# Optimization experiments

Hardware: AMD Instinct MI355X
Metric: run time of the kernel (lower is better)

## Reference

```python
import jax, jax.numpy as jnp
import numpy as np

N = 50000
E = 800000
IN_DIM = 128
OUT_DIM = 128


def setup_inputs() -> dict:
    key = jax.random.key(0)
    k1, k2, k3, k4 = jax.random.split(key, 4)
    x = jax.random.normal(k1, (N, IN_DIM), dtype=jnp.float32)
    edge_index = jax.random.randint(k2, (2, E), 0, N, dtype=jnp.int64)
    # Linear(in_dim*2, out_dim) params
    W = jax.random.normal(k3, (2 * IN_DIM, OUT_DIM), dtype=jnp.float32) * (1.0 / np.sqrt(2 * IN_DIM))
    b = jax.random.normal(k4, (OUT_DIM,), dtype=jnp.float32) * 0.01
    return {"x": x, "edge_index": edge_index, "W": W, "b": b}


def reference(x, edge_index, W, b):
    src, dst = edge_index[0], edge_index[1]
    diff = x[src] - x[dst]                              # (E, C)
    # segment-max over destination nodes; empty segments get -inf identity
    seg_max = jax.ops.segment_max(diff, dst, num_segments=N)  # (N, C)
    counts = jax.ops.segment_sum(jnp.ones((E,), dtype=jnp.int32), dst, num_segments=N)
    # original code leaves zeros for nodes with no incoming edges
    max_diff = jnp.where((counts > 0)[:, None], seg_max, jnp.zeros_like(seg_max))
    x_cat = jnp.concatenate([x, max_diff], axis=-1)     # (N, 2C)
    return x_cat @ W + b
```

## Files before the change

kernel.cpp:

```cpp
#include <hip/hip_runtime.h>
#include <math.h>

#define NN 50000
#define NE 800000
#define CD 128
#define NBKT 49
#define CAP 24576
#define SLICE 4096
#define EBLK 196
#define CASTB 2048
#define NBLK2 1563

typedef __attribute__((ext_vector_type(8))) short short8;
typedef __attribute__((ext_vector_type(4))) float f32x4;


__device__ inline unsigned pack2bf(float lo, float hi) {
    unsigned a = __float_as_uint(lo), b = __float_as_uint(hi);
    a = (a + 0x7fffu + ((a >> 16) & 1u)) >> 16;
    b = (b + 0x7fffu + ((b >> 16) & 1u)) & 0xffff0000u;
    return a | b;
}

__device__ inline unsigned short f2bf(float f) {
    unsigned u = __float_as_uint(f);
    return (unsigned short)((u + 0x7fffu + ((u >> 16) & 1u)) >> 16);
}

__device__ inline void fmax8(float* m, uint4 v) {
    m[0] = fmaxf(m[0], __uint_as_float(v.x << 16));
    m[1] = fmaxf(m[1], __uint_as_float(v.x & 0xffff0000u));
    m[2] = fmaxf(m[2], __uint_as_float(v.y << 16));
    m[3] = fmaxf(m[3], __uint_as_float(v.y & 0xffff0000u));
    m[4] = fmaxf(m[4], __uint_as_float(v.z << 16));
    m[5] = fmaxf(m[5], __uint_as_float(v.z & 0xffff0000u));
    m[6] = fmaxf(m[6], __uint_as_float(v.w << 16));
    m[7] = fmaxf(m[7], __uint_as_float(v.w & 0xffff0000u));
}


__global__ __launch_bounds__(256) void prep5_k(const int* __restrict__ ei,
                                               const float* __restrict__ x,
                                               const float* __restrict__ W,
                                               int* __restrict__ cur,
                                               int* __restrict__ ovfn,
                                               unsigned* __restrict__ ovf,
                                               unsigned* __restrict__ csr,
                                               unsigned* __restrict__ xb,
                                               unsigned short* __restrict__ wt) {
    int b = blockIdx.x;
    int t = threadIdx.x;
    if (b < EBLK) {
        __shared__ int hist[64];
        __shared__ int curs[64];
        int e0 = b * SLICE;
        int e1 = min(NE, e0 + SLICE);
        if (t < 64) hist[t] = 0;
        __syncthreads();
        for (int e = e0 + t; e < e1; e += 256)
            atomicAdd(&hist[((unsigned)ei[NE + e]) >> 10], 1);
        __syncthreads();
        if (t < NBKT) curs[t] = atomicAdd(&cur[t], hist[t]);
        __syncthreads();
        for (int e = e0 + t; e < e1; e += 256) {
            int d = ei[NE + e];
            int s = ei[e];
            int bin = ((unsigned)d) >> 10;
            int p = atomicAdd(&curs[bin], 1);
            if (p < CAP) {
                csr[(size_t)bin * CAP + p] = ((unsigned)s << 10) | (unsigned)(d & 1023);
            } else {
                int op = atomicAdd(ovfn, 1);
                ovf[op] = ((unsigned)s << 16) | (unsigned)d;
            }
        }
    } else {
        int tid0 = (b - EBLK) * 256 + t;
        for (int i = tid0; i < NN * CD / 4; i += CASTB * 256) {
            float4 v = ((const float4*)x)[i];
            uint2 r;
            r.x = pack2bf(v.x, v.y);
            r.y = pack2bf(v.z, v.w);
            ((uint2*)xb)[i] = r;
        }
        for (int i = tid0; i < 2 * CD * CD; i += CASTB * 256) {
            int n = i >> 8, k = i & 255;
            wt[(size_t)n * 256 + k] = f2bf(W[(size_t)k * 128 + n]);
        }
    }
}


__global__ __launch_bounds__(256) void fused_k(const unsigned* __restrict__ xb,
                                               const int* __restrict__ cur,
                                               const int* __restrict__ ovfn,
                                               const unsigned* __restrict__ ovf,
                                               const unsigned* __restrict__ csr,
                                               const short* __restrict__ wt,
                                               const float* __restrict__ bias,
                                               float* __restrict__ out) {
    __shared__ unsigned short idx[32][72];
    __shared__ unsigned short amx[32][136];
    __shared__ int lcnt[32];
    __shared__ int spill[512];
    __shared__ int spn;

    int t = threadIdx.x;
    int B = blockIdx.x;
    int qb = B >> 5;
    int sub = B & 31;
    int nbase = B * 32;

    if (t < 32) lcnt[t] = 0;
    if (t == 32) spn = 0;
    __syncthreads();

    int cnt = min(cur[qb], CAP);
    const unsigned* base = csr + (size_t)qb * CAP;
    for (int i = t; i < cnt; i += 256) {
        unsigned w = base[i];
        if ((int)((w >> 5) & 31) == sub) {
            int ln = (int)(w & 31u);
            int s = (int)(w >> 10);
            int pos = atomicAdd(&lcnt[ln], 1);
            if (pos < 64) idx[ln][pos] = (unsigned short)s;
            else { int sp = atomicAdd(&spn, 1); if (sp < 512) spill[sp] = (s << 6) | ln; }
        }
    }
    int ovN = min(ovfn[0], NE);
    for (int i = t; i < ovN; i += 256) {
        unsigned w = ovf[i];
        int d = (int)(w & 0xffffu);
        if ((d >> 5) == B) {
            int ln = d & 31;
            int s = (int)(w >> 16);
            int pos = atomicAdd(&lcnt[ln], 1);
            if (pos < 64) idx[ln][pos] = (unsigned short)s;
            else { int sp = atomicAdd(&spn, 1); if (sp < 512) spill[sp] = (s << 6) | ln; }
        }
    }
    __syncthreads();

    int w = t >> 6, lane = t & 63;
    int q = lane >> 4, c = lane & 15;
    int sN = min(spn, 512);
#pragma unroll 1
    for (int j = 0; j < 2; j++) {
        int ln = w * 8 + j * 4 + q;
        int node = nbase + ln;
        int lc = lcnt[ln];
        int lim = min(lc, 64);
        float m[8];
#pragma unroll
        for (int i = 0; i < 8; i++) m[i] = -INFINITY;

        for (int bb = 0; bb < lim; bb += 8) {
            uint4 pk = *(const uint4*)&idx[ln][bb];
            int s0 = (int)(pk.x & 0xffffu), s1 = (int)(pk.x >> 16);
            int s2 = (int)(pk.y & 0xffffu), s3 = (int)(pk.y >> 16);
            int s4 = (int)(pk.z & 0xffffu), s5 = (int)(pk.z >> 16);
            int s6 = (int)(pk.w & 0xffffu), s7 = (int)(pk.w >> 16);
            if (bb + 8 <= lim) {
                fmax8(m, *(const uint4*)(xb + (size_t)s0 * 64 + c * 4));
                fmax8(m, *(const uint4*)(xb + (size_t)s1 * 64 + c * 4));
                fmax8(m, *(const uint4*)(xb + (size_t)s2 * 64 + c * 4));
                fmax8(m, *(const uint4*)(xb + (size_t)s3 * 64 + c * 4));
                fmax8(m, *(const uint4*)(xb + (size_t)s4 * 64 + c * 4));
                fmax8(m, *(const uint4*)(xb + (size_t)s5 * 64 + c * 4));
                fmax8(m, *(const uint4*)(xb + (size_t)s6 * 64 + c * 4));
                fmax8(m, *(const uint4*)(xb + (size_t)s7 * 64 + c * 4));
            } else {
                if (bb + 0 < lim) fmax8(m, *(const uint4*)(xb + (size_t)s0 * 64 + c * 4));
                if (bb + 1 < lim) fmax8(m, *(const uint4*)(xb + (size_t)s1 * 64 + c * 4));
                if (bb + 2 < lim) fmax8(m, *(const uint4*)(xb + (size_t)s2 * 64 + c * 4));
                if (bb + 3 < lim) fmax8(m, *(const uint4*)(xb + (size_t)s3 * 64 + c * 4));
                if (bb + 4 < lim) fmax8(m, *(const uint4*)(xb + (size_t)s4 * 64 + c * 4));
                if (bb + 5 < lim) fmax8(m, *(const uint4*)(xb + (size_t)s5 * 64 + c * 4));
                if (bb + 6 < lim) fmax8(m, *(const uint4*)(xb + (size_t)s6 * 64 + c * 4));
                if (bb + 7 < lim) fmax8(m, *(const uint4*)(xb + (size_t)s7 * 64 + c * 4));
            }
        }
        for (int i = 0; i < sN; i++) {
            int sw = spill[i];
            if ((sw & 63) == ln)
                fmax8(m, *(const uint4*)(xb + (size_t)(sw >> 6) * 64 + c * 4));
        }
        uint4 r = make_uint4(0u, 0u, 0u, 0u);
        if (lc > 0) {
            uint4 xd = *(const uint4*)(xb + (size_t)node * 64 + c * 4);
            float d0 = m[0] - __uint_as_float(xd.x << 16);
            float d1 = m[1] - __uint_as_float(xd.x & 0xffff0000u);
            float d2 = m[2] - __uint_as_float(xd.y << 16);
            float d3 = m[3] - __uint_as_float(xd.y & 0xffff0000u);
            float d4 = m[4] - __uint_as_float(xd.z << 16);
            float d5 = m[5] - __uint_as_float(xd.z & 0xffff0000u);
            float d6 = m[6] - __uint_as_float(xd.w << 16);
            float d7 = m[7] - __uint_as_float(xd.w & 0xffff0000u);
            r.x = pack2bf(d0, d1);
            r.y = pack2bf(d2, d3);
            r.z = pack2bf(d4, d5);
            r.w = pack2bf(d6, d7);
        }
        *(uint4*)&amx[ln][c * 8] = r;
    }
    __syncthreads();

    int mm = lane & 15, g4 = lane >> 4;
    int rt = w & 1, ch = w >> 1;
    int r0 = nbase + rt * 16;
    int row = r0 + mm;
    bool rowok = row < NN;

    f32x4 acc[4];
#pragma unroll
    for (int ct = 0; ct < 4; ct++) {
        float bv = bias[ch * 64 + ct * 16 + mm];
        acc[ct] = (f32x4){bv, bv, bv, bv};
    }

    const short* xbs = (const short*)xb;
#pragma unroll
    for (int kc = 0; kc < 8; kc++) {
        int k0 = kc * 32;
        short8 a;
        if (kc < 4) {
            a = (short8){0, 0, 0, 0, 0, 0, 0, 0};
            if (rowok) a = *(const short8*)(xbs + (size_t)row * 128 + k0 + g4 * 8);
        } else {
            a = *(const short8*)&amx[rt * 16 + mm][(k0 - 128) + g4 * 8];
        }
#pragma unroll
        for (int ct = 0; ct < 4; ct++) {
            short8 bb = *(const short8*)(wt + (size_t)(ch * 64 + ct * 16 + mm) * 256 + k0 + g4 * 8);
            acc[ct] = __builtin_amdgcn_mfma_f32_16x16x32_bf16(a, bb, acc[ct], 0, 0, 0);
        }
    }

#pragma unroll
    for (int ct = 0; ct < 4; ct++) {
#pragma unroll
        for (int i = 0; i < 4; i++) {
            int rr = r0 + g4 * 4 + i;
            if (rr < NN) out[(size_t)rr * 128 + ch * 64 + ct * 16 + mm] = acc[ct][i];
        }
    }
}


extern "C" void kernel_launch(void* const* d_in, const int* in_sizes, int n_in,
                              void* d_out, int out_size, void* d_ws, size_t ws_size,
                              hipStream_t stream) {
    const float* x = (const float*)d_in[0];
    const int* ei = (const int*)d_in[1];
    const float* W = (const float*)d_in[2];
    const float* bias = (const float*)d_in[3];
    float* out = (float*)d_out;

    int* wsi = (int*)d_ws;
    int* cur   = wsi;
    int* ovfn  = wsi + 64;
    unsigned* ovf = (unsigned*)(wsi + 80);
    unsigned* csr = (unsigned*)(wsi + 800080);
    unsigned* xb  = (unsigned*)(wsi + 2004304);
    unsigned short* wt = (unsigned short*)(wsi + 5204304);

    hipMemsetAsync(cur, 0, 80 * sizeof(int), stream);

    prep5_k<<<EBLK + CASTB, 256, 0, stream>>>(ei, x, W, cur, ovfn, ovf, csr, xb, wt);
    fused_k<<<NBLK2, 256, 0, stream>>>(xb, cur, ovfn, ovf, csr, (const short*)wt,
                                       bias, out);
}
```

Baseline: 200.8 us.

## Add second-level rebin pass so fused kernel reads only its own edges

```diff
diff --git a/kernel.cpp b/kernel.cpp
--- a/kernel.cpp
+++ b/kernel.cpp
@@ -10,6 +10,7 @@
 #define EBLK 196
 #define CASTB 2048
 #define NBLK2 1563
+#define SUBCAP 768
 
 typedef __attribute__((ext_vector_type(8))) short short8;
 typedef __attribute__((ext_vector_type(4))) float f32x4;
@@ -27,15 +28,9 @@
     return (unsigned short)((u + 0x7fffu + ((u >> 16) & 1u)) >> 16);
 }
 
-__device__ inline void fmax8(float* m, uint4 v) {
-    m[0] = fmaxf(m[0], __uint_as_float(v.x << 16));
-    m[1] = fmaxf(m[1], __uint_as_float(v.x & 0xffff0000u));
-    m[2] = fmaxf(m[2], __uint_as_float(v.y << 16));
-    m[3] = fmaxf(m[3], __uint_as_float(v.y & 0xffff0000u));
-    m[4] = fmaxf(m[4], __uint_as_float(v.z << 16));
-    m[5] = fmaxf(m[5], __uint_as_float(v.z & 0xffff0000u));
-    m[6] = fmaxf(m[6], __uint_as_float(v.w << 16));
-    m[7] = fmaxf(m[7], __uint_as_float(v.w & 0xffff0000u));
+__device__ inline void fmax2(float& a, float& b, unsigned v) {
+    a = fmaxf(a, __uint_as_float(v << 16));
+    b = fmaxf(b, __uint_as_float(v & 0xffff0000u));
 }
 
 
@@ -91,11 +86,47 @@
 }
 
 
+__global__ __launch_bounds__(256) void rebin_k(const int* __restrict__ cur,
+                                               const unsigned* __restrict__ csr,
+                                               int* __restrict__ subcur,
+                                               int* __restrict__ ovfn2,
+                                               unsigned* __restrict__ ovf2,
+                                               unsigned* __restrict__ csr2) {
+    __shared__ int hist[32];
+    __shared__ int curs[32];
+    int b = blockIdx.x, t = threadIdx.x;
+    int q = b >> 3, s = b & 7;
+    int cnt = min(cur[q], CAP);
+    int i0 = (cnt * s) >> 3, i1 = (cnt * (s + 1)) >> 3;
+    if (t < 32) hist[t] = 0;
+    __syncthreads();
+    const unsigned* base = csr + (size_t)q * CAP;
+    for (int i = i0 + t; i < i1; i += 256)
+        atomicAdd(&hist[(base[i] >> 5) & 31], 1);
+    __syncthreads();
+    if (t < 32) curs[t] = atomicAdd(&subcur[q * 32 + t], hist[t]);
+    __syncthreads();
+    for (int i = i0 + t; i < i1; i += 256) {
+        unsigned w = base[i];
+        int sub = (int)((w >> 5) & 31u);
+        int p = atomicAdd(&curs[sub], 1);
+        if (p < SUBCAP) {
+            csr2[(size_t)(q * 32 + sub) * SUBCAP + p] = ((w >> 10) << 5) | (w & 31u);
+        } else {
+            int op = atomicAdd(ovfn2, 1);
+            ovf2[op] = ((w >> 10) << 16) | (unsigned)(q * 1024 + (int)(w & 1023u));
+        }
+    }
+}
+
+
 __global__ __launch_bounds__(256) void fused_k(const unsigned* __restrict__ xb,
-                                               const int* __restrict__ cur,
+                                               const int* __restrict__ subcur,
                                                const int* __restrict__ ovfn,
                                                const unsigned* __restrict__ ovf,
-                                               const unsigned* __restrict__ csr,
+                                               const int* __restrict__ ovfn2,
+                                               const unsigned* __restrict__ ovf2,
+                                               const unsigned* __restrict__ csr2,
                                                const short* __restrict__ wt,
                                                const float* __restrict__ bias,
                                                float* __restrict__ out) {
@@ -107,25 +138,21 @@
 
     int t = threadIdx.x;
     int B = blockIdx.x;
-    int qb = B >> 5;
-    int sub = B & 31;
     int nbase = B * 32;
 
     if (t < 32) lcnt[t] = 0;
     if (t == 32) spn = 0;
     __syncthreads();
 
-    int cnt = min(cur[qb], CAP);
-    const unsigned* base = csr + (size_t)qb * CAP;
+    int cnt = min(subcur[B], SUBCAP);
+    const unsigned* base = csr2 + (size_t)B * SUBCAP;
     for (int i = t; i < cnt; i += 256) {
         unsigned w = base[i];
-        if ((int)((w >> 5) & 31) == sub) {
-            int ln = (int)(w & 31u);
-            int s = (int)(w >> 10);
-            int pos = atomicAdd(&lcnt[ln], 1);
-            if (pos < 64) idx[ln][pos] = (unsigned short)s;
-            else { int sp = atomicAdd(&spn, 1); if (sp < 512) spill[sp] = (s << 6) | ln; }
-        }
+        int ln = (int)(w & 31u);
+        int s = (int)(w >> 5);
+        int pos = atomicAdd(&lcnt[ln], 1);
+        if (pos < 64) idx[ln][pos] = (unsigned short)s;
+        else { int sp = atomicAdd(&spn, 1); if (sp < 512) spill[sp] = (s << 6) | ln; }
     }
     int ovN = min(ovfn[0], NE);
     for (int i = t; i < ovN; i += 256) {
@@ -139,69 +166,77 @@
             else { int sp = atomicAdd(&spn, 1); if (sp < 512) spill[sp] = (s << 6) | ln; }
         }
     }
+    int ovN2 = min(ovfn2[0], NE);
+    for (int i = t; i < ovN2; i += 256) {
+        unsigned w = ovf2[i];
+        int d = (int)(w & 0xffffu);
+        if ((d >> 5) == B) {
+            int ln = d & 31;
+            int s = (int)(w >> 16);
+            int pos = atomicAdd(&lcnt[ln], 1);
+            if (pos < 64) idx[ln][pos] = (unsigned short)s;
+            else { int sp = atomicAdd(&spn, 1); if (sp < 512) spill[sp] = (s << 6) | ln; }
+        }
+    }
     __syncthreads();
 
     int w = t >> 6, lane = t & 63;
-    int q = lane >> 4, c = lane & 15;
+    int q4 = lane >> 4, c = lane & 15;
     int sN = min(spn, 512);
 #pragma unroll 1
-    for (int j = 0; j < 2; j++) {
-        int ln = w * 8 + j * 4 + q;
-        int node = nbase + ln;
-        int lc = lcnt[ln];
-        int lim = min(lc, 64);
-        float m[8];
-#pragma unroll
-        for (int i = 0; i < 8; i++) m[i] = -INFINITY;
-
-        for (int bb = 0; bb < lim; bb += 8) {
-            uint4 pk = *(const uint4*)&idx[ln][bb];
-            int s0 = (int)(pk.x & 0xffffu), s1 = (int)(pk.x >> 16);
-            int s2 = (int)(pk.y & 0xffffu), s3 = (int)(pk.y >> 16);
-            int s4 = (int)(pk.z & 0xffffu), s5 = (int)(pk.z >> 16);
-            int s6 = (int)(pk.w & 0xffffu), s7 = (int)(pk.w >> 16);
-            if (bb + 8 <= lim) {
-                fmax8(m, *(const uint4*)(xb + (size_t)s0 * 64 + c * 4));
-                fmax8(m, *(const uint4*)(xb + (size_t)s1 * 64 + c * 4));
-                fmax8(m, *(const uint4*)(xb + (size_t)s2 * 64 + c * 4));
-                fmax8(m, *(const uint4*)(xb + (size_t)s3 * 64 + c * 4));
-                fmax8(m, *(const uint4*)(xb + (size_t)s4 * 64 + c * 4));
-                fmax8(m, *(const uint4*)(xb + (size_t)s5 * 64 + c * 4));
-                fmax8(m, *(const uint4*)(xb + (size_t)s6 * 64 + c * 4));
-                fmax8(m, *(const uint4*)(xb + (size_t)s7 * 64 + c * 4));
-            } else {
-                if (bb + 0 < lim) fmax8(m, *(const uint4*)(xb + (size_t)s0 * 64 + c * 4));
-                if (bb + 1 < lim) fmax8(m, *(const uint4*)(xb + (size_t)s1 * 64 + c * 4));
-                if (bb + 2 < lim) fmax8(m, *(const uint4*)(xb + (size_t)s2 * 64 + c * 4));
-                if (bb + 3 < lim) fmax8(m, *(const uint4*)(xb + (size_t)s3 * 64 + c * 4));
-                if (bb + 4 < lim) fmax8(m, *(const uint4*)(xb + (size_t)s4 * 64 + c * 4));
-                if (bb + 5 < lim) fmax8(m, *(const uint4*)(xb + (size_t)s5 * 64 + c * 4));
-                if (bb + 6 < lim) fmax8(m, *(const uint4*)(xb + (size_t)s6 * 64 + c * 4));
-                if (bb + 7 < lim) fmax8(m, *(const uint4*)(xb + (size_t)s7 * 64 + c * 4));
+    for (int cb = 0; cb < 4; cb++) {
+        const unsigned* xcb = xb + cb * 16 + c;
+#pragma unroll 1
+        for (int j = 0; j < 2; j++) {
+            int ln = w * 8 + j * 4 + q4;
+            int node = nbase + ln;
+            int lc = lcnt[ln];
+            int lim = min(lc, 64);
+            float m0 = -INFINITY, m1 = -INFINITY;
+
+            for (int bb = 0; bb < lim; bb += 8) {
+                uint4 pk = *(const uint4*)&idx[ln][bb];
+                int s0 = (int)(pk.x & 0xffffu), s1 = (int)(pk.x >> 16);
+                int s2 = (int)(pk.y & 0xffffu), s3 = (int)(pk.y >> 16);
+                int s4 = (int)(pk.z & 0xffffu), s5 = (int)(pk.z >> 16);
+                int s6 = (int)(pk.w & 0xffffu), s7 = (int)(pk.w >> 16);
+                if (bb + 8 <= lim) {
+                    unsigned v0 = xcb[(size_t)s0 * 64];
+                    unsigned v1 = xcb[(size_t)s1 * 64];
+                    unsigned v2 = xcb[(size_t)s2 * 64];
+                    unsigned v3 = xcb[(size_t)s3 * 64];
+                    unsigned v4 = xcb[(size_t)s4 * 64];
+                    unsigned v5 = xcb[(size_t)s5 * 64];
+                    unsigned v6 = xcb[(size_t)s6 * 64];
+                    unsigned v7 = xcb[(size_t)s7 * 64];
+                    fmax2(m0, m1, v0); fmax2(m0, m1, v1);
+                    fmax2(m0, m1, v2); fmax2(m0, m1, v3);
+                    fmax2(m0, m1, v4); fmax2(m0, m1, v5);
+                    fmax2(m0, m1, v6); fmax2(m0, m1, v7);
+                } else {
+                    if (bb + 0 < lim) fmax2(m0, m1, xcb[(size_t)s0 * 64]);
+                    if (bb + 1 < lim) fmax2(m0, m1, xcb[(size_t)s1 * 64]);
+                    if (bb + 2 < lim) fmax2(m0, m1, xcb[(size_t)s2 * 64]);
+                    if (bb + 3 < lim) fmax2(m0, m1, xcb[(size_t)s3 * 64]);
+                    if (bb + 4 < lim) fmax2(m0, m1, xcb[(size_t)s4 * 64]);
+                    if (bb + 5 < lim) fmax2(m0, m1, xcb[(size_t)s5 * 64]);
+                    if (bb + 6 < lim) fmax2(m0, m1, xcb[(size_t)s6 * 64]);
+                    if (bb + 7 < lim) fmax2(m0, m1, xcb[(size_t)s7 * 64]);
+                }
             }
-        }
-        for (int i = 0; i < sN; i++) {
-            int sw = spill[i];
-            if ((sw & 63) == ln)
-                fmax8(m, *(const uint4*)(xb + (size_t)(sw >> 6) * 64 + c * 4));
-        }
-        uint4 r = make_uint4(0u, 0u, 0u, 0u);
-        if (lc > 0) {
-            uint4 xd = *(const uint4*)(xb + (size_t)node * 64 + c * 4);
-            float d0 = m[0] - __uint_as_float(xd.x << 16);
-            float d1 = m[1] - __uint_as_float(xd.x & 0xffff0000u);
-            float d2 = m[2] - __uint_as_float(xd.y << 16);
-            float d3 = m[3] - __uint_as_float(xd.y & 0xffff0000u);
-            float d4 = m[4] - __uint_as_float(xd.z << 16);
-            float d5 = m[5] - __uint_as_float(xd.z & 0xffff0000u);
-            float d6 = m[6] - __uint_as_float(xd.w << 16);
-            float d7 = m[7] - __uint_as_float(xd.w & 0xffff0000u);
-            r.x = pack2bf(d0, d1);
-            r.y = pack2bf(d2, d3);
-            r.z = pack2bf(d4, d5);
-            r.w = pack2bf(d6, d7);
-        }
-        *(uint4*)&amx[ln][c * 8] = r;
+            for (int i = 0; i < sN; i++) {
+                int sw = spill[i];
+                if ((sw & 63) == ln) fmax2(m0, m1, xcb[(size_t)(sw >> 6) * 64]);
+            }
+            unsigned r = 0u;
+            if (lc > 0) {
+                unsigned xd = xcb[(size_t)node * 64];
+                float d0 = m0 - __uint_as_float(xd << 16);
+                float d1 = m1 - __uint_as_float(xd & 0xffff0000u);
+                r = pack2bf(d0, d1);
+            }
+            *(unsigned*)&amx[ln][cb * 32 + c * 2] = r;
+        }
     }
     __syncthreads();
 
@@ -257,16 +292,21 @@
     float* out = (float*)d_out;
 
     int* wsi = (int*)d_ws;
-    int* cur   = wsi;
-    int* ovfn  = wsi + 64;
-    unsigned* ovf = (unsigned*)(wsi + 80);
-    unsigned* csr = (unsigned*)(wsi + 800080);
-    unsigned* xb  = (unsigned*)(wsi + 2004304);
-    unsigned short* wt = (unsigned short*)(wsi + 5204304);
-
-    hipMemsetAsync(cur, 0, 80 * sizeof(int), stream);
+    int* cur    = wsi;
+    int* ovfn   = wsi + 64;
+    int* subcur = wsi + 80;
+    int* ovfn2  = wsi + 1648;
+    unsigned* ovf  = (unsigned*)(wsi + 2048);
+    unsigned* csr  = (unsigned*)(wsi + 802048);
+    unsigned* csr2 = (unsigned*)(wsi + 2006272);
+    unsigned* ovf2 = (unsigned*)(wsi + 3210496);
+    unsigned* xb   = (unsigned*)(wsi + 4010496);
+    unsigned short* wt = (unsigned short*)(wsi + 7210496);
+
+    hipMemsetAsync(cur, 0, 2048 * sizeof(int), stream);
 
     prep5_k<<<EBLK + CASTB, 256, 0, stream>>>(ei, x, W, cur, ovfn, ovf, csr, xb, wt);
-    fused_k<<<NBLK2, 256, 0, stream>>>(xb, cur, ovfn, ovf, csr, (const short*)wt,
-                                       bias, out);
-}
+    rebin_k<<<NBKT * 8, 256, 0, stream>>>(cur, csr, subcur, ovfn2, ovf2, csr2);
+    fused_k<<<NBLK2, 256, 0, stream>>>(xb, subcur, ovfn, ovf, ovfn2, ovf2, csr2,
+                                       (const short*)wt, bias, out);
+}
```

New measurement: 199.9 us. About the same (-0.5%).
